# Kernel tuning notes

Measured on AMD Instinct MI355X. Metric: run time of the kernel, lower is better.

The kernel has to match this reference:

```python
import jax, jax.numpy as jnp
import numpy as np

B, S, E, OUT = 16, 2048, 256, 256


def setup_inputs() -> dict:
    key = jax.random.key(0)
    k1, k2 = jax.random.split(key)
    x = jax.random.normal(k1, (B, S, E), dtype=jnp.float32)
    alpha = jnp.float32(0.5)  # nn.Parameter(torch.tensor(0.5))
    W = jax.random.normal(k2, (OUT, E), dtype=jnp.float32) * (1.0 / np.sqrt(E))
    b = jnp.zeros((OUT,), dtype=jnp.float32)
    return {"x": x, "alpha\u0308".replace("\u0308", ""): alpha, "W": W, "b": b}


def reference(x, alpha, W, b):
    # Gaussian energy-well self-attention: q = k = v = x, shape (B, S, E)
    # cdist(q, k, p=2)**2 == ||q||^2 + ||k||^2 - 2 q.k
    sq = jnp.sum(x * x, axis=-1)                                   # (B, S)
    d2 = sq[:, :, None] + sq[:, None, :] - 2.0 * jnp.einsum(
        "bse,bte->bst", x, x)                                      # (B, S, S)
    d2 = jnp.maximum(d2, 0.0)
    weights = jnp.exp(-alpha * d2)                                 # (B, S, S)
    weights = jax.nn.softmax(weights, axis=-1)
    attn = jnp.einsum("bst,bte->bse", weights, x)                  # (B, S, E)
    pooled = attn.mean(axis=1)                                     # (B, E)
    return pooled @ W.T + b                                        # (B, OUT)
```

## Files before the change

kernel.cpp:

```cpp
#include <hip/hip_runtime.h>
#include <hip/hip_bf16.h>

#define NB 16
#define NS 2048
#define NE 256
#define NOUT 256
#define CAP 49152
#define RCAP 384

typedef __attribute__((ext_vector_type(4))) float f32x4;
typedef __attribute__((ext_vector_type(8))) short s16x8;
typedef __attribute__((ext_vector_type(4))) short s16x4;
typedef unsigned int u32;
typedef unsigned long long u64;

__device__ __forceinline__ short bf16rn(float f) {
  unsigned u = __builtin_bit_cast(unsigned, f);
  u += 0x7FFFu + ((u >> 16) & 1u);
  return (short)(u >> 16);
}
__device__ __forceinline__ float bf16f(short s) {
  unsigned u = ((unsigned)(unsigned short)s) << 16;
  return __builtin_bit_cast(float, u);
}
__device__ __forceinline__ void gld_lds16(const void* g, void* l) {
  __builtin_amdgcn_global_load_lds(
      (const __attribute__((address_space(1))) u32*)g,
      (__attribute__((address_space(3))) u32*)l, 16, 0, 0);
}

__global__ __launch_bounds__(256) void prep_kernel(const float* __restrict__ x,
                                                   short* __restrict__ xbf,
                                                   float* __restrict__ sq,
                                                   u32* __restrict__ counter) {
  if (blockIdx.x == 0 && threadIdx.x == 0) *counter = 0u;
  int row = blockIdx.x * 4 + (threadIdx.x >> 6);
  int lane = threadIdx.x & 63;
  f32x4 v = *(const f32x4*)(x + (size_t)row * NE + lane * 4);
  s16x4 p;
  p[0] = bf16rn(v.x); p[1] = bf16rn(v.y); p[2] = bf16rn(v.z); p[3] = bf16rn(v.w);
  *(s16x4*)(xbf + (size_t)row * NE + lane * 4) = p;
  float s = v.x * v.x + v.y * v.y + v.z * v.z + v.w * v.w;
#pragma unroll
  for (int off = 32; off; off >>= 1) s += __shfl_xor(s, off);
  if (lane == 0) sq[row] = s;
}

__global__ __launch_bounds__(256, 2) void gram_kernel(
    const short* __restrict__ xbf, const float* __restrict__ sqg,
    const float* __restrict__ alpha_p, float* __restrict__ rpart,
    u32* __restrict__ counter, u32* __restrict__ records) {
  __shared__ __align__(16) char smem[32768];
  __shared__ u32 rec_meta[RCAP];
  __shared__ float rec_e[RCAP];
  __shared__ u32 rec_cnt, rec_gbase;

  const int tid = threadIdx.x;
  const int lane = tid & 63;
  const int wid = tid >> 6;
  const int lrow = lane & 15, lq = lane >> 4;

  const int nbid = (blockIdx.x & 7) * 128 + (blockIdx.x >> 3);
  const int b = nbid >> 6;
  const int strip = (nbid >> 2) & 15;
  const int quad = nbid & 3;
  const int rowbase = strip * 128;
  const int colbase = quad * 512;
  const char* xc = (const char*)(xbf + (size_t)b * NS * NE);
  const float alpha = alpha_p[0];
  const float nal = -alpha;
  const float thresh = 17.328680f / alpha;

  if (tid == 0) rec_cnt = 0u;

  s16x8 af[2][8];
#pragma unroll
  for (int m = 0; m < 2; ++m) {
    const char* arow = xc + (size_t)(rowbase + wid * 32 + m * 16 + lrow) * 512;
#pragma unroll
    for (int ks = 0; ks < 8; ++ks)
      af[m][ks] = *(const s16x8*)(arow + ks * 64 + lq * 16);
  }
  float rr[2][4], minrr = 3.4e38f;
#pragma unroll
  for (int m = 0; m < 2; ++m)
#pragma unroll
    for (int j = 0; j < 4; ++j) {
      rr[m][j] = sqg[b * NS + rowbase + wid * 32 + m * 16 + lq * 4 + j];
      minrr = fminf(minrr, rr[m][j]);
    }

  const int swzl = ((lane & 7) * 16) ^ ((lane >> 3) << 4);
  auto stageB = [&](int bt, int c, char* buf) {
    const char* base = xc + (size_t)(colbase + bt * 128 + wid * 32 + (lane >> 3)) * 512 +
                       c * 128 + swzl;
    char* dst = buf + wid * 4096 + lane * 16;
#pragma unroll
    for (int i = 0; i < 4; ++i) {
      gld_lds16(base + (size_t)(i * 8) * 512, dst + i * 1024);
    }
  };

  f32x4 acc[2][8];
#pragma unroll
  for (int m = 0; m < 2; ++m)
#pragma unroll
    for (int n = 0; n < 8; ++n) acc[m][n] = (f32x4){0.f, 0.f, 0.f, 0.f};
  float prs[2][4] = {{0.f, 0.f, 0.f, 0.f}, {0.f, 0.f, 0.f, 0.f}};

  stageB(0, 0, smem);
  __syncthreads();

#pragma unroll 1
  for (int bt = 0; bt < 4; ++bt) {
#pragma unroll
    for (int c = 0; c < 4; ++c) {
      if (!(bt == 3 && c == 3)) {
        int btn = (c == 3) ? bt + 1 : bt;
        stageB(btn, (c + 1) & 3, smem + (((c + 1) & 1) ? 16384 : 0));
      }
      const char* buf = smem + ((c & 1) ? 16384 : 0);
#pragma unroll
      for (int ks = 0; ks < 2; ++ks) {
        s16x8 bv[8];
#pragma unroll
        for (int n = 0; n < 8; ++n) {
          int col = n * 16 + lrow;
          bv[n] = *(const s16x8*)(buf + col * 128 +
                                  ((ks * 64 + lq * 16) ^ ((col & 7) << 4)));
        }
#pragma unroll
        for (int m = 0; m < 2; ++m)
#pragma unroll
          for (int n = 0; n < 8; ++n)
            acc[m][n] = __builtin_amdgcn_mfma_f32_16x16x32_bf16(
                af[m][c * 2 + ks], bv[n], acc[m][n], 0, 0, 0);
      }

      if (c == 3) {
        const int btg = quad * 4 + bt;
        float cc[8], mincc = 3.4e38f;
#pragma unroll
        for (int n = 0; n < 8; ++n) {
          cc[n] = sqg[b * NS + btg * 128 + n * 16 + lrow];
          mincc = fminf(mincc, cc[n]);
        }
        float maxg = -3.4e38f;
#pragma unroll
        for (int m = 0; m < 2; ++m)
#pragma unroll
          for (int n = 0; n < 8; ++n)
#pragma unroll
            for (int j = 0; j < 4; ++j) maxg = fmaxf(maxg, acc[m][n][j]);
        bool fast = (minrr + mincc - 2.f * maxg > thresh);
        if (__all(fast)) {
#pragma unroll
          for (int m = 0; m < 2; ++m)
#pragma unroll
            for (int j = 0; j < 4; ++j) prs[m][j] += 8.0f;
        } else {
#pragma unroll
          for (int m = 0; m < 2; ++m) {
#pragma unroll
            for (int j = 0; j < 4; ++j) {
              float rj = rr[m][j];
#pragma unroll
              for (int n = 0; n < 8; ++n) {
                float d2 = fmaxf(fmaf(-2.f, acc[m][n][j], rj + cc[n]), 0.f);
                float w0 = __expf(nal * d2);
                float e = __expf(w0);
                prs[m][j] += e;
                if (d2 < thresh) {
                  u32 idx = atomicAdd(&rec_cnt, 1u);
                  if (idx < RCAP) {
                    int srow = rowbase + wid * 32 + m * 16 + lq * 4 + j;
                    int tcol = btg * 128 + n * 16 + lrow;
                    rec_meta[idx] = ((u32)srow << 11) | (u32)tcol;
                    rec_e[idx] = e;
                  }
                }
              }
            }
          }
        }
#pragma unroll
        for (int m = 0; m < 2; ++m)
#pragma unroll
          for (int n = 0; n < 8; ++n) acc[m][n] = (f32x4){0.f, 0.f, 0.f, 0.f};
      }
      __syncthreads();
    }
  }

#pragma unroll
  for (int m = 0; m < 2; ++m)
#pragma unroll
    for (int j = 0; j < 4; ++j) {
      float v = prs[m][j];
      v += __shfl_xor(v, 1);
      v += __shfl_xor(v, 2);
      v += __shfl_xor(v, 4);
      v += __shfl_xor(v, 8);
      if (lrow == 0)
        rpart[(size_t)(b * 4 + quad) * NS + rowbase + wid * 32 + m * 16 +
              lq * 4 + j] = v;
    }

  u32 cnt = rec_cnt;
  if (cnt > RCAP) cnt = RCAP;
  if (cnt) {
    if (tid == 0) rec_gbase = atomicAdd(counter, cnt);
    __syncthreads();
    u32 gb = rec_gbase;
    for (u32 i = tid; i < cnt; i += 256) {
      u32 g = gb + i;
      if (g < CAP) {
        records[2 * g] = ((u32)b << 22) | rec_meta[i];
        records[2 * g + 1] = __builtin_bit_cast(u32, rec_e[i]);
      }
    }
  }
}

__global__ __launch_bounds__(1024) void finale_kernel(
    const short* __restrict__ xbf, const float* __restrict__ rpart,
    const u32* __restrict__ counter, const u32* __restrict__ records,
    const float* __restrict__ W, const float* __restrict__ bias,
    float* __restrict__ out) {
  __shared__ float rinv_l[NS];
  __shared__ float c_l[NS];
  __shared__ float red[32 * 256];
  __shared__ float pooled_l[NE];
  const int b = blockIdx.x;
  const int tid = threadIdx.x;
  const int lane = tid & 63;
  const int wv = tid >> 6;

  float inv_acc = 0.f;
#pragma unroll
  for (int k = 0; k < 2; ++k) {
    int row = k * 1024 + tid;
    float r = rpart[(size_t)(4 * b + 0) * NS + row] +
              rpart[(size_t)(4 * b + 1) * NS + row] +
              rpart[(size_t)(4 * b + 2) * NS + row] +
              rpart[(size_t)(4 * b + 3) * NS + row];
    float inv = 1.0f / r;
    rinv_l[row] = inv;
    inv_acc += inv;
  }
#pragma unroll
  for (int off = 32; off; off >>= 1) inv_acc += __shfl_xor(inv_acc, off);
  if (lane == 0) red[wv] = inv_acc;
  __syncthreads();
  float tot = 0.f;
#pragma unroll
  for (int g = 0; g < 16; ++g) tot += red[g];
#pragma unroll
  for (int k = 0; k < 2; ++k) c_l[k * 1024 + tid] = tot;
  __syncthreads();

  u32 cnt = *counter;
  if (cnt > CAP) cnt = CAP;
  for (u32 i = tid; i < cnt; i += 1024) {
    u32 meta = records[2 * i];
    if ((int)(meta >> 22) != b) continue;
    float e = __builtin_bit_cast(float, records[2 * i + 1]);
    int s = (meta >> 11) & 2047, t = meta & 2047;
    atomicAdd(&c_l[t], (e - 1.0f) * rinv_l[s]);
  }
  __syncthreads();

  const short* xb = xbf + (size_t)b * NS * NE;
  const int e8 = (lane & 31) * 8;
  const int tgrp = wv * 2 + (lane >> 5);
  float acc[8] = {0.f, 0.f, 0.f, 0.f, 0.f, 0.f, 0.f, 0.f};
#pragma unroll 4
  for (int tt = 0; tt < 64; ++tt) {
    int t = tgrp * 64 + tt;
    float cv = c_l[t];
    s16x8 v = *(const s16x8*)(xb + (size_t)t * NE + e8);
#pragma unroll
    for (int j = 0; j < 8; ++j) acc[j] = fmaf(cv, bf16f(v[j]), acc[j]);
  }
#pragma unroll
  for (int j = 0; j < 8; ++j) red[tgrp * 256 + e8 + j] = acc[j];
  __syncthreads();
  if (tid < NE) {
    float s = 0.f;
#pragma unroll
    for (int g = 0; g < 32; ++g) s += red[g * 256 + tid];
    pooled_l[tid] = s * (1.0f / NS);
  }
  __syncthreads();

  if (tid < NOUT) {
    const f32x4* wr4 = (const f32x4*)(W + (size_t)tid * NE);
    float a = bias[tid];
#pragma unroll 8
    for (int e = 0; e < 64; ++e) {
      f32x4 w4 = wr4[e];
      a += pooled_l[e * 4 + 0] * w4.x + pooled_l[e * 4 + 1] * w4.y +
           pooled_l[e * 4 + 2] * w4.z + pooled_l[e * 4 + 3] * w4.w;
    }
    out[b * NOUT + tid] = a;
  }
}

extern "C" void kernel_launch(void* const* d_in, const int* in_sizes, int n_in,
                              void* d_out, int out_size, void* d_ws, size_t ws_size,
                              hipStream_t stream) {
  const float* x = (const float*)d_in[0];
  const float* alpha = (const float*)d_in[1];
  const float* W = (const float*)d_in[2];
  const float* bias = (const float*)d_in[3];
  float* out = (float*)d_out;

  u32* counter = (u32*)d_ws;
  float* sq = (float*)(counter + 32);
  float* rpart = sq + NB * NS;
  u32* records = (u32*)(rpart + 4 * NB * NS);
  short* xbf = (short*)(records + 2 * CAP);

  prep_kernel<<<NB * NS / 4, 256, 0, stream>>>(x, xbf, sq, counter);
  gram_kernel<<<1024, 256, 0, stream>>>(xbf, sq, alpha, rpart, counter, records);
  finale_kernel<<<NB, 1024, 0, stream>>>(xbf, rpart, counter, records, W, bias,
                                         out);
}
```

Before: 154.9 us.

## Split finale into cfix, pooled-partial and output kernels; raise gram occupancy

```diff
diff --git a/kernel.cpp b/kernel.cpp
--- a/kernel.cpp
+++ b/kernel.cpp
@@ -46,7 +46,7 @@
   if (lane == 0) sq[row] = s;
 }
 
-__global__ __launch_bounds__(256, 2) void gram_kernel(
+__global__ __launch_bounds__(256, 4) void gram_kernel(
     const short* __restrict__ xbf, const float* __restrict__ sqg,
     const float* __restrict__ alpha_p, float* __restrict__ rpart,
     u32* __restrict__ counter, u32* __restrict__ records) {
@@ -222,15 +222,12 @@
   }
 }
 
-__global__ __launch_bounds__(1024) void finale_kernel(
-    const short* __restrict__ xbf, const float* __restrict__ rpart,
-    const u32* __restrict__ counter, const u32* __restrict__ records,
-    const float* __restrict__ W, const float* __restrict__ bias,
-    float* __restrict__ out) {
+__global__ __launch_bounds__(512) void cfix_kernel(
+    const float* __restrict__ rpart, const u32* __restrict__ counter,
+    const u32* __restrict__ records, float* __restrict__ cws) {
   __shared__ float rinv_l[NS];
   __shared__ float c_l[NS];
-  __shared__ float red[32 * 256];
-  __shared__ float pooled_l[NE];
+  __shared__ float red[8];
   const int b = blockIdx.x;
   const int tid = threadIdx.x;
   const int lane = tid & 63;
@@ -238,8 +235,8 @@
 
   float inv_acc = 0.f;
 #pragma unroll
-  for (int k = 0; k < 2; ++k) {
-    int row = k * 1024 + tid;
+  for (int k = 0; k < 4; ++k) {
+    int row = k * 512 + tid;
     float r = rpart[(size_t)(4 * b + 0) * NS + row] +
               rpart[(size_t)(4 * b + 1) * NS + row] +
               rpart[(size_t)(4 * b + 2) * NS + row] +
@@ -254,14 +251,14 @@
   __syncthreads();
   float tot = 0.f;
 #pragma unroll
-  for (int g = 0; g < 16; ++g) tot += red[g];
-#pragma unroll
-  for (int k = 0; k < 2; ++k) c_l[k * 1024 + tid] = tot;
+  for (int g = 0; g < 8; ++g) tot += red[g];
+#pragma unroll
+  for (int k = 0; k < 4; ++k) c_l[k * 512 + tid] = tot;
   __syncthreads();
 
   u32 cnt = *counter;
   if (cnt > CAP) cnt = CAP;
-  for (u32 i = tid; i < cnt; i += 1024) {
+  for (u32 i = tid; i < cnt; i += 512) {
     u32 meta = records[2 * i];
     if ((int)(meta >> 22) != b) continue;
     float e = __builtin_bit_cast(float, records[2 * i + 1]);
@@ -269,41 +266,62 @@
     atomicAdd(&c_l[t], (e - 1.0f) * rinv_l[s]);
   }
   __syncthreads();
-
-  const short* xb = xbf + (size_t)b * NS * NE;
-  const int e8 = (lane & 31) * 8;
-  const int tgrp = wv * 2 + (lane >> 5);
+#pragma unroll
+  for (int k = 0; k < 4; ++k) {
+    int t = k * 512 + tid;
+    cws[(size_t)b * NS + t] = c_l[t];
+  }
+}
+
+__global__ __launch_bounds__(256) void pooledp_kernel(
+    const short* __restrict__ xbf, const float* __restrict__ cws,
+    float* __restrict__ pooled_part) {
+  __shared__ float red[8 * 256];
+  const int slice = blockIdx.x;
+  const int b = blockIdx.y;
+  const int t0 = slice * 256;
+  const short* xb = xbf + ((size_t)b * NS + t0) * NE;
+  const float* cb = cws + (size_t)b * NS + t0;
+  const int g = threadIdx.x >> 5;
+  const int e8 = (threadIdx.x & 31) * 8;
   float acc[8] = {0.f, 0.f, 0.f, 0.f, 0.f, 0.f, 0.f, 0.f};
 #pragma unroll 4
-  for (int tt = 0; tt < 64; ++tt) {
-    int t = tgrp * 64 + tt;
-    float cv = c_l[t];
+  for (int tt = 0; tt < 32; ++tt) {
+    int t = g + tt * 8;
+    float cv = cb[t];
     s16x8 v = *(const s16x8*)(xb + (size_t)t * NE + e8);
 #pragma unroll
     for (int j = 0; j < 8; ++j) acc[j] = fmaf(cv, bf16f(v[j]), acc[j]);
   }
 #pragma unroll
-  for (int j = 0; j < 8; ++j) red[tgrp * 256 + e8 + j] = acc[j];
-  __syncthreads();
-  if (tid < NE) {
-    float s = 0.f;
-#pragma unroll
-    for (int g = 0; g < 32; ++g) s += red[g * 256 + tid];
-    pooled_l[tid] = s * (1.0f / NS);
-  }
-  __syncthreads();
-
-  if (tid < NOUT) {
-    const f32x4* wr4 = (const f32x4*)(W + (size_t)tid * NE);
-    float a = bias[tid];
+  for (int j = 0; j < 8; ++j) red[g * 256 + e8 + j] = acc[j];
+  __syncthreads();
+  float s = 0.f;
+#pragma unroll
+  for (int g2 = 0; g2 < 8; ++g2) s += red[g2 * 256 + threadIdx.x];
+  pooled_part[((size_t)b * 8 + slice) * NE + threadIdx.x] = s;
+}
+
+__global__ __launch_bounds__(256) void out_kernel(
+    const float* __restrict__ pooled_part, const float* __restrict__ W,
+    const float* __restrict__ bias, float* __restrict__ out) {
+  __shared__ float pl[NE];
+  const int b = blockIdx.x, o = threadIdx.x;
+  float s = 0.f;
+#pragma unroll
+  for (int sl = 0; sl < 8; ++sl)
+    s += pooled_part[((size_t)b * 8 + sl) * NE + o];
+  pl[o] = s * (1.0f / NS);
+  __syncthreads();
+  const f32x4* wr4 = (const f32x4*)(W + (size_t)o * NE);
+  float a = bias[o];
 #pragma unroll 8
-    for (int e = 0; e < 64; ++e) {
-      f32x4 w4 = wr4[e];
-      a += pooled_l[e * 4 + 0] * w4.x + pooled_l[e * 4 + 1] * w4.y +
-           pooled_l[e * 4 + 2] * w4.z + pooled_l[e * 4 + 3] * w4.w;
-    }
-    out[b * NOUT + tid] = a;
-  }
+  for (int e = 0; e < 64; ++e) {
+    f32x4 w4 = wr4[e];
+    a += pl[e * 4 + 0] * w4.x + pl[e * 4 + 1] * w4.y + pl[e * 4 + 2] * w4.z +
+         pl[e * 4 + 3] * w4.w;
+  }
+  out[b * NOUT + o] = a;
 }
 
 extern "C" void kernel_launch(void* const* d_in, const int* in_sizes, int n_in,
@@ -319,10 +337,13 @@
   float* sq = (float*)(counter + 32);
   float* rpart = sq + NB * NS;
   u32* records = (u32*)(rpart + 4 * NB * NS);
-  short* xbf = (short*)(records + 2 * CAP);
+  float* cws = (float*)(records + 2 * CAP);
+  float* pooled_part = cws + NB * NS;
+  short* xbf = (short*)(pooled_part + NB * 8 * NE);
 
   prep_kernel<<<NB * NS / 4, 256, 0, stream>>>(x, xbf, sq, counter);
   gram_kernel<<<1024, 256, 0, stream>>>(xbf, sq, alpha, rpart, counter, records);
-  finale_kernel<<<NB, 1024, 0, stream>>>(xbf, rpart, counter, records, W, bias,
-                                         out);
-}
+  cfix_kernel<<<NB, 512, 0, stream>>>(rpart, counter, records, cws);
+  pooledp_kernel<<<dim3(8, NB), 256, 0, stream>>>(xbf, cws, pooled_part);
+  out_kernel<<<NB, 256, 0, stream>>>(pooled_part, W, bias, out);
+}
```

New measurement: 195.0 us. +25.9%, slower.
